# Optimization experiments

Measured on AMD Instinct MI355X. Metric: run time of the kernel, lower is better.

The kernel has to match this reference:

```python
import jax, jax.numpy as jnp
from jax import lax
import numpy as np

V, EMB, ELMO, WORD, H, B, R, L = 11322, 300, 1024, 512, 512, 32, 10, 20


def setup_inputs():
    key = jax.random.key(0)
    ks = jax.random.split(key, 24)

    def n(k, shape, s=0.02):
        return jax.random.normal(k, shape, dtype=jnp.float32) * s

    inp = {}
    inp["ques"] = jax.random.randint(ks[0], (B, R, L), 0, V)
    inp["hist"] = jax.random.randint(ks[1], (B, R, 2 * L), 0, V)
    inp["ques_len"] = jax.random.randint(ks[2], (B, R), 1, L + 1)
    inp["hist_len"] = jax.random.randint(ks[3], (B, R), 1, 2 * L + 1)
    inp["img_feat"] = n(ks[4], (B, 36, 2048), 1.0)
    inp["v_relations"] = n(ks[5], (B, 36, 36, 512), 1.0)
    inp["w_emb"] = n(ks[6], (V, EMB))          # GloVe/numberbatch table
    inp["elmo_emb"] = n(ks[7], (V, ELMO))      # frozen ELMo table
    inp["Wc"] = n(ks[8], (WORD, ELMO))         # embed_change Linear
    inp["bc"] = jnp.zeros((WORD,), jnp.float32)
    IN0 = EMB + WORD                            # LSTM layer-0 input size = 812
    names = ["q_Wih0", "q_Whh0", "q_b0", "q_Wih1", "q_Whh1", "q_b1",
             "h_Wih0", "h_Whh0", "h_b0", "h_Wih1", "h_Whh1", "h_b1"]
    shapes = [(4 * H, IN0), (4 * H, H), (4 * H,), (4 * H, H), (4 * H, H), (4 * H,)] * 2
    for i, (nm, sh) in enumerate(zip(names, shapes)):
        inp[nm] = n(ks[9 + i], sh, 0.04)
    return inp


def lstm_layer(x, Wih, Whh, b):
    # x: [N, T, In] -> all hidden states [N, T, H]; PyTorch gate order i,f,g,o
    N = x.shape[0]
    Hh = Whh.shape[1]
    xproj = jnp.einsum('nti,gi->ntg', x, Wih) + b  # [N, T, 4H]

    def step(carry, xp):
        h, c = carry
        gates = xp + h @ Whh.T
        i, f, g, o = jnp.split(gates, 4, axis=-1)
        c = jax.nn.sigmoid(f) * c + jax.nn.sigmoid(i) * jnp.tanh(g)
        h = jax.nn.sigmoid(o) * jnp.tanh(c)
        return (h, c), h

    h0 = jnp.zeros((N, Hh), x.dtype)
    _, hs = lax.scan(step, (h0, h0), jnp.swapaxes(xproj, 0, 1))
    return jnp.swapaxes(hs, 0, 1)


def encode(tokens, lens, w_emb, elmo_emb, Wc, bc, Wih0, Whh0, b0, Wih1, Whh1, b1):
    # Embedding lookup + elmo->word projection, 2-layer LSTM, take h at t = len-1
    Ntok = tokens.shape[0]
    emb = w_emb[tokens]                         # [N, T, 300]
    elmo = elmo_emb[tokens] @ Wc.T + bc         # [N, T, 512] (dropout off: eval)
    x = jnp.concatenate([emb, elmo], axis=-1)   # [N, T, 812]
    h1 = lstm_layer(x, Wih0, Whh0, b0)
    h2 = lstm_layer(h1, Wih1, Whh1, b1)
    return h2[jnp.arange(Ntok), lens - 1]       # DynamicRNN: last valid hidden


def reference(ques, hist, ques_len, hist_len, img_feat, v_relations, w_emb, elmo_emb, Wc, bc,
              q_Wih0, q_Whh0, q_b0, q_Wih1, q_Whh1, q_b1,
              h_Wih0, h_Whh0, h_b0, h_Wih1, h_Whh1, h_b1):
    Bq, Rr, Ll = ques.shape
    ques_embed = encode(ques.reshape(Bq * Rr, Ll), ques_len.reshape(-1),
                        w_emb, elmo_emb, Wc, bc,
                        q_Wih0, q_Whh0, q_b0, q_Wih1, q_Whh1, q_b1).reshape(Bq, Rr, -1)
    hist_embed = encode(hist.reshape(Bq * Rr, 2 * Ll), hist_len.reshape(-1),
                        w_emb, elmo_emb, Wc, bc,
                        h_Wih0, h_Whh0, h_b0, h_Wih1, h_Whh1, h_b1).reshape(Bq, Rr, -1)
    # Vectorized form of the Python double loop + pad_sequence:
    # f_history[b, i, j] = hist_embed[b, j] if j <= i else 0   -> [B, R, R, H]
    tri = jnp.tril(jnp.ones((Rr, Rr), hist_embed.dtype))
    f_history = hist_embed[:, None, :, :] * tri[None, :, :, None]
    # masks exactly as t_rel.abs().sum(-1).bool() on the broadcast tensors
    m = (jnp.abs(f_history).sum(-1) != 0)       # [B, R, R]
    # t_rel[b,i,j,k,:] = f_history[b,i,j,:] zeroed where tmp (=f_history[b,i,k]) is zero
    t_rel = f_history[:, :, :, None, :] * m[:, :, None, :, None]
    tmp = f_history[:, :, None, :, :] * m[:, :, :, None, None]
    text_rel = jnp.concatenate([t_rel, tmp], axis=-1)  # [B, R, R, R, 2H]
    return ques_embed, text_rel
```

## Files before the change

### kernel.cpp

```cpp
#include <hip/hip_runtime.h>
#include <math.h>

#define NSEQ 320
#define HDIM 512
#define G4   2048
#define EMBD 300
#define ELMOD 1024
#define XPAD 832

typedef __attribute__((ext_vector_type(8))) short bf16x8;
typedef __attribute__((ext_vector_type(4))) float f32x4;
typedef unsigned short ushort_t;

__device__ __forceinline__ float sigmoidf_(float x) { return 1.0f / (1.0f + expf(-x)); }

__device__ __forceinline__ ushort_t f2bf(float f) {
    unsigned u = __float_as_uint(f);
    u = (u + 0x7FFFu + ((u >> 16) & 1u)) >> 16;
    return (ushort_t)u;
}
__device__ __forceinline__ float bf2f(ushort_t u) {
    return __uint_as_float(((unsigned)u) << 16);
}
__device__ __forceinline__ unsigned pack2(float a, float b) {
    return (unsigned)f2bf(a) | ((unsigned)f2bf(b) << 16);
}

__global__ __launch_bounds__(256) void conv_bf16_kernel(
    const float* __restrict__ src, int srcCols,
    ushort_t* __restrict__ dst, int dstStride, int dstOff,
    int fillCols)
{
    int c = blockIdx.x * 256 + threadIdx.x;
    int r = blockIdx.y;
    if (c >= fillCols) return;
    float v = (c < srcCols) ? src[(size_t)r * srcCols + c] : 0.0f;
    dst[(size_t)r * dstStride + dstOff + c] = f2bf(v);
}

__global__ __launch_bounds__(128) void emb_gather_kernel(
    const int* __restrict__ tok, const float* __restrict__ w_emb,
    ushort_t* __restrict__ Xb)
{
    int n = blockIdx.x;
    int t = threadIdx.x;
    ushort_t* dst = Xb + (size_t)n * XPAD;
    if (t < 75) {
        const float4* src = (const float4*)(w_emb + (size_t)tok[n] * EMBD);
        float4 v = src[t];
        dst[4*t+0] = f2bf(v.x); dst[4*t+1] = f2bf(v.y);
        dst[4*t+2] = f2bf(v.z); dst[4*t+3] = f2bf(v.w);
    } else if (t >= 108) {
        dst[812 + (t - 108)] = 0;
    }
}

__global__ __launch_bounds__(256) void gemm_ff_kernel(
    const ushort_t* __restrict__ Ab, const float* __restrict__ Af,
    const int* __restrict__ tok, int strideA,
    const ushort_t* __restrict__ W, const float* __restrict__ bias,
    ushort_t* __restrict__ C, int strideC, int K)
{
    __shared__ ushort_t As[64 * 40];
    __shared__ ushort_t Bs[64 * 40];
    const int m0 = blockIdx.y * 64;
    const int n0 = blockIdx.x * 64;
    const int tid = threadIdx.x;
    const int r  = tid >> 2;
    const int kq = (tid & 3) << 3;

    const ushort_t* arow_b = nullptr;
    const float*    arow_f = nullptr;
    if (Af) arow_f = Af + (size_t)tok[m0 + r] * strideA + kq;
    else    arow_b = Ab + (size_t)(m0 + r) * strideA + kq;
    const ushort_t* brow = W + (size_t)(n0 + r) * K + kq;

    const int lane = tid & 63;
    const int w = tid >> 6;
    const int wm = w & 1, wn = w >> 1;
    const int kc = (lane >> 4) << 3;

    f32x4 acc[2][2];
    #pragma unroll
    for (int f = 0; f < 2; ++f)
        #pragma unroll
        for (int g = 0; g < 2; ++g)
            acc[f][g] = (f32x4){0.f, 0.f, 0.f, 0.f};

    for (int k0 = 0; k0 < K; k0 += 32) {
        if (Af) {
            float4 v0 = ((const float4*)(arow_f + k0))[0];
            float4 v1 = ((const float4*)(arow_f + k0))[1];
            uint4 p; p.x = pack2(v0.x, v0.y); p.y = pack2(v0.z, v0.w);
            p.z = pack2(v1.x, v1.y); p.w = pack2(v1.z, v1.w);
            *(uint4*)&As[r*40 + kq] = p;
        } else {
            *(uint4*)&As[r*40 + kq] = *(const uint4*)(arow_b + k0);
        }
        *(uint4*)&Bs[r*40 + kq] = *(const uint4*)(brow + k0);
        __syncthreads();
        bf16x8 af[2], bfr[2];
        #pragma unroll
        for (int f = 0; f < 2; ++f)
            af[f] = *(const bf16x8*)&As[(wm*32 + f*16 + (lane & 15))*40 + kc];
        #pragma unroll
        for (int g = 0; g < 2; ++g)
            bfr[g] = *(const bf16x8*)&Bs[(wn*32 + g*16 + (lane & 15))*40 + kc];
        #pragma unroll
        for (int f = 0; f < 2; ++f)
            #pragma unroll
            for (int g = 0; g < 2; ++g)
                acc[f][g] = __builtin_amdgcn_mfma_f32_16x16x32_bf16(af[f], bfr[g], acc[f][g], 0, 0, 0);
        __syncthreads();
    }

    #pragma unroll
    for (int f = 0; f < 2; ++f) {
        #pragma unroll
        for (int g = 0; g < 2; ++g) {
            int col = n0 + wn*32 + g*16 + (lane & 15);
            float bv = bias[col];
            #pragma unroll
            for (int i = 0; i < 4; ++i) {
                int row = m0 + wm*32 + f*16 + ((lane >> 4) << 2) + i;
                C[(size_t)row * strideC + col] = f2bf(acc[f][g][i] + bv);
            }
        }
    }
}

struct Cell {
    const ushort_t* A;
    const ushort_t* B;
    const ushort_t* xp;
    const float* bias;
    float* c;
    ushort_t* hA;
    ushort_t* hB;
    float* hlast;
    const int* lens;
    int t, K, strideHA, xpRowStride;
};
struct CellPack { Cell cells[4]; };

__global__ __launch_bounds__(256) void lstm_superstep_kernel(CellPack P)
{
    const Cell cl = P.cells[blockIdx.z];
    const int j0 = blockIdx.x * 16;
    const int n0 = blockIdx.y * 64;
    __shared__ ushort_t As[64 * 40];
    __shared__ ushort_t Bs[64 * 40];
    __shared__ float Gt[64][68];

    const int tid = threadIdx.x;
    const int r  = tid >> 2;
    const int kq = (tid & 3) << 3;
    const int K = cl.K;

    const ushort_t* arow = cl.A + (size_t)(n0 + r) * K + kq;
    const ushort_t* brow = cl.B + (size_t)((r >> 4) * HDIM + j0 + (r & 15)) * K + kq;

    const int lane = tid & 63;
    const int w = tid >> 6;
    const int wm = w & 1, wn = w >> 1;
    const int kc = (lane >> 4) << 3;

    f32x4 acc[2][2];
    #pragma unroll
    for (int f = 0; f < 2; ++f)
        #pragma unroll
        for (int g = 0; g < 2; ++g)
            acc[f][g] = (f32x4){0.f, 0.f, 0.f, 0.f};

    for (int k0 = 0; k0 < K; k0 += 32) {
        *(uint4*)&As[r*40 + kq] = *(const uint4*)(arow + k0);
        *(uint4*)&Bs[r*40 + kq] = *(const uint4*)(brow + k0);
        __syncthreads();
        bf16x8 af[2], bfr[2];
        #pragma unroll
        for (int f = 0; f < 2; ++f)
            af[f] = *(const bf16x8*)&As[(wm*32 + f*16 + (lane & 15))*40 + kc];
        #pragma unroll
        for (int g = 0; g < 2; ++g)
            bfr[g] = *(const bf16x8*)&Bs[(wn*32 + g*16 + (lane & 15))*40 + kc];
        #pragma unroll
        for (int f = 0; f < 2; ++f)
            #pragma unroll
            for (int g = 0; g < 2; ++g)
                acc[f][g] = __builtin_amdgcn_mfma_f32_16x16x32_bf16(af[f], bfr[g], acc[f][g], 0, 0, 0);
        __syncthreads();
    }

    #pragma unroll
    for (int f = 0; f < 2; ++f)
        #pragma unroll
        for (int g = 0; g < 2; ++g)
            #pragma unroll
            for (int i = 0; i < 4; ++i)
                Gt[wm*32 + f*16 + ((lane >> 4) << 2) + i][wn*32 + g*16 + (lane & 15)] = acc[f][g][i];
    __syncthreads();

    #pragma unroll
    for (int q = 0; q < 4; ++q) {
        int p = tid + q * 256;
        int nl = p >> 4, jj = p & 15;
        int n = n0 + nl, j = j0 + jj;
        float gi = Gt[nl][jj],      gf = Gt[nl][16 + jj];
        float gg = Gt[nl][32 + jj], go = Gt[nl][48 + jj];
        if (cl.xp) {
            const ushort_t* xr = cl.xp + (size_t)n * cl.xpRowStride;
            gi += bf2f(xr[j]);          gf += bf2f(xr[HDIM + j]);
            gg += bf2f(xr[2*HDIM + j]); go += bf2f(xr[3*HDIM + j]);
        } else {
            gi += cl.bias[j];          gf += cl.bias[HDIM + j];
            gg += cl.bias[2*HDIM + j]; go += cl.bias[3*HDIM + j];
        }
        size_t ix = (size_t)n * HDIM + j;
        float c = cl.c[ix];
        c = sigmoidf_(gf) * c + sigmoidf_(gi) * tanhf(gg);
        float h = sigmoidf_(go) * tanhf(c);
        cl.c[ix] = c;
        cl.hA[(size_t)n * cl.strideHA + j] = f2bf(h);
        if (cl.hB) cl.hB[(size_t)n * 1024 + j] = f2bf(h);
        if (cl.hlast && (cl.lens[n] - 1 == cl.t)) cl.hlast[ix] = h;
    }
}

__global__ __launch_bounds__(64) void nz_kernel(
    const float* __restrict__ he, int* __restrict__ nz)
{
    int rr = blockIdx.x;
    int lane = threadIdx.x;
    const float* row = he + (size_t)rr * HDIM;
    bool any = false;
    for (int k = lane; k < HDIM; k += 64) any |= (row[k] != 0.0f);
    unsigned long long b = __ballot(any);
    if (lane == 0) nz[rr] = (b != 0ull) ? 1 : 0;
}

__global__ __launch_bounds__(256) void expand_kernel(
    const float* __restrict__ he, const int* __restrict__ nz,
    float* __restrict__ out)
{
    int blk = blockIdx.x;
    int k = blk % 10;
    int j = (blk / 10) % 10;
    int i = (blk / 100) % 10;
    int b = blk / 1000;
    int tid = threadIdx.x;
    float4* o = (float4*)(out + (size_t)blk * 1024);
    float4 z; z.x = z.y = z.z = z.w = 0.0f;
    if (tid < 128) {
        bool m = (j <= i) && (k <= i) && (nz[b*10 + k] != 0);
        float4 v = m ? ((const float4*)(he + (size_t)(b*10 + j) * HDIM))[tid] : z;
        o[tid] = v;
    } else {
        int c = tid - 128;
        bool m = (k <= i) && (j <= i) && (nz[b*10 + j] != 0);
        float4 v = m ? ((const float4*)(he + (size_t)(b*10 + k) * HDIM))[c] : z;
        o[128 + c] = v;
    }
}

extern "C" void kernel_launch(void* const* d_in, const int* in_sizes, int n_in,
                              void* d_out, int out_size, void* d_ws, size_t ws_size,
                              hipStream_t stream)
{
    (void)in_sizes; (void)n_in; (void)out_size; (void)ws_size;
    const int* ques     = (const int*)d_in[0];
    const int* hist     = (const int*)d_in[1];
    const int* ques_len = (const int*)d_in[2];
    const int* hist_len = (const int*)d_in[3];
    const float* w_emb  = (const float*)d_in[6];
    const float* elmo   = (const float*)d_in[7];
    const float* Wc     = (const float*)d_in[8];
    const float* bc     = (const float*)d_in[9];

    char* ws = (char*)d_ws;
    size_t off = 0;
    auto alloc = [&](size_t bytes) { char* p = ws + off; off += (bytes + 15) & ~(size_t)15; return p; };
    ushort_t* XP0bf   = (ushort_t*)alloc((size_t)19200 * G4 * 2);
    ushort_t* Xb      = (ushort_t*)alloc((size_t)19200 * XPAD * 2);
    ushort_t* Wcb     = (ushort_t*)alloc((size_t)HDIM * ELMOD * 2);
    ushort_t* Wih0b[2], *Whh0b[2], *Wcat[2];
    for (int s = 0; s < 2; ++s) {
        Wih0b[s] = (ushort_t*)alloc((size_t)G4 * XPAD * 2);
        Whh0b[s] = (ushort_t*)alloc((size_t)G4 * HDIM * 2);
        Wcat[s]  = (ushort_t*)alloc((size_t)G4 * ELMOD * 2);
    }
    char* state_base = ws + off;
    ushort_t* h0buf[2][2];
    ushort_t* acat[2][2];
    float* cbuf[2][2];
    for (int s = 0; s < 2; ++s)
        for (int p = 0; p < 2; ++p) h0buf[s][p] = (ushort_t*)alloc((size_t)NSEQ * HDIM * 2);
    for (int s = 0; s < 2; ++s)
        for (int p = 0; p < 2; ++p) acat[s][p] = (ushort_t*)alloc((size_t)NSEQ * ELMOD * 2);
    for (int s = 0; s < 2; ++s)
        for (int l = 0; l < 2; ++l) cbuf[s][l] = (float*)alloc((size_t)NSEQ * HDIM * 4);
    size_t state_bytes = (ws + off) - state_base;
    float* he = (float*)alloc((size_t)NSEQ * HDIM * 4);
    int* nzb  = (int*)alloc(NSEQ * 4);

    float* out = (float*)d_out;
    float* ques_embed = out;
    float* text_rel   = out + (size_t)NSEQ * HDIM;

    const int rowoff[2] = {0, 6400};
    const int TT[2] = {20, 40};
    const int* toks[2] = {ques, hist};
    const int* lens[2] = {ques_len, hist_len};

    conv_bf16_kernel<<<dim3(4, HDIM), 256, 0, stream>>>(Wc, ELMOD, Wcb, ELMOD, 0, ELMOD);
    for (int s = 0; s < 2; ++s) {
        const float* Wih0 = (const float*)d_in[10 + 6*s];
        const float* Whh0 = (const float*)d_in[11 + 6*s];
        const float* Wih1 = (const float*)d_in[13 + 6*s];
        const float* Whh1 = (const float*)d_in[14 + 6*s];
        conv_bf16_kernel<<<dim3(4, G4), 256, 0, stream>>>(Wih0, 812, Wih0b[s], XPAD, 0, XPAD);
        conv_bf16_kernel<<<dim3(2, G4), 256, 0, stream>>>(Whh0, HDIM, Whh0b[s], HDIM, 0, HDIM);
        conv_bf16_kernel<<<dim3(2, G4), 256, 0, stream>>>(Wih1, HDIM, Wcat[s], ELMOD, 0, HDIM);
        conv_bf16_kernel<<<dim3(2, G4), 256, 0, stream>>>(Whh1, HDIM, Wcat[s], ELMOD, HDIM, HDIM);
    }

    for (int s = 0; s < 2; ++s) {
        int Ntok = NSEQ * TT[s];
        ushort_t* XbS = Xb + (size_t)rowoff[s] * XPAD;
        emb_gather_kernel<<<Ntok, 128, 0, stream>>>(toks[s], w_emb, XbS);
        gemm_ff_kernel<<<dim3(HDIM/64, Ntok/64), 256, 0, stream>>>(
            nullptr, elmo, toks[s], ELMOD, Wcb, bc, XbS + EMBD, XPAD, ELMOD);
        const float* b0 = (const float*)d_in[12 + 6*s];
        gemm_ff_kernel<<<dim3(G4/64, Ntok/64), 256, 0, stream>>>(
            XbS, nullptr, nullptr, XPAD, Wih0b[s], b0,
            XP0bf + (size_t)rowoff[s] * G4, G4, XPAD);
    }

    hipMemsetAsync(state_base, 0, state_bytes, stream);

    for (int ss = 0; ss <= 40; ++ss) {
        int par = ss & 1;
        CellPack P;
        int nc = 0;
        for (int s = 0; s < 2; ++s) {
            int T = TT[s];
            const float* b1 = (const float*)d_in[15 + 6*s];
            if (ss < T) {
                Cell& c = P.cells[nc++];
                c.A = h0buf[s][par]; c.B = Whh0b[s];
                c.xp = XP0bf + ((size_t)rowoff[s] + ss) * G4;
                c.xpRowStride = T * G4;
                c.bias = nullptr;
                c.c = cbuf[s][0];
                c.hA = h0buf[s][par ^ 1]; c.strideHA = HDIM;
                c.hB = acat[s][par ^ 1];
                c.hlast = nullptr; c.lens = lens[s];
                c.t = ss; c.K = HDIM;
            }
            if (ss >= 1 && ss <= T) {
                Cell& c = P.cells[nc++];
                c.A = acat[s][par]; c.B = Wcat[s];
                c.xp = nullptr; c.xpRowStride = 0;
                c.bias = b1;
                c.c = cbuf[s][1];
                c.hA = acat[s][par ^ 1] + HDIM; c.strideHA = ELMOD;
                c.hB = nullptr;
                c.hlast = s ? he : ques_embed; c.lens = lens[s];
                c.t = ss - 1; c.K = ELMOD;
            }
        }
        if (nc == 0) continue;
        lstm_superstep_kernel<<<dim3(HDIM/16, NSEQ/64, nc), 256, 0, stream>>>(P);
    }

    nz_kernel<<<NSEQ, 64, 0, stream>>>(he, nzb);
    expand_kernel<<<32000, 256, 0, stream>>>(he, nzb, text_rel);
}
```

Before: 1.192 ms.

## Replace per-timestep LSTM launches with a persistent kernel and grid barriers

Replaces the 41 per-superstep LSTM launches with one persistent kernel of 256 blocks, one group of 64 blocks per (sequence, layer) cell. The two cells of each sequence are synchronised between steps by an atomic-counter spin barrier. Cell state stays in registers, the A and B operands are loaded straight from global memory into registers with double buffering instead of going through LDS, and gate columns are arranged so each lane's i/f/g/o values are exchanged with shuffles. The aim is to remove launch overhead and the c-state round-trips to memory. In exchange it relies on all blocks being co-resident, and the spin loop has a timeout that could break correctness if it ever fires.

New measurement: 1.896 ms. 59.0% more time.

```diff
diff --git a/kernel.cpp b/kernel.cpp
--- a/kernel.cpp
+++ b/kernel.cpp
@@ -129,101 +129,141 @@
     }
 }
 
-struct Cell {
-    const ushort_t* A;
+struct PCell {
+    const ushort_t* A0; const ushort_t* A1;
     const ushort_t* B;
     const ushort_t* xp;
     const float* bias;
-    float* c;
-    ushort_t* hA;
-    ushort_t* hB;
+    ushort_t* O0; ushort_t* O1;
     float* hlast;
     const int* lens;
-    int t, K, strideHA, xpRowStride;
+    int K, T, layer;
 };
-struct CellPack { Cell cells[4]; };
-
-__global__ __launch_bounds__(256) void lstm_superstep_kernel(CellPack P)
-{
-    const Cell cl = P.cells[blockIdx.z];
-    const int j0 = blockIdx.x * 16;
-    const int n0 = blockIdx.y * 64;
-    __shared__ ushort_t As[64 * 40];
-    __shared__ ushort_t Bs[64 * 40];
-    __shared__ float Gt[64][68];
-
-    const int tid = threadIdx.x;
-    const int r  = tid >> 2;
-    const int kq = (tid & 3) << 3;
-    const int K = cl.K;
-
-    const ushort_t* arow = cl.A + (size_t)(n0 + r) * K + kq;
-    const ushort_t* brow = cl.B + (size_t)((r >> 4) * HDIM + j0 + (r & 15)) * K + kq;
-
+struct PPack { PCell cell[4]; };
+
+__global__ __launch_bounds__(256) void lstm_persist_kernel(PPack P, int* ctrs)
+{
+    const int cellId = blockIdx.x >> 6;
+    const int blk    = blockIdx.x & 63;
+    const PCell c = P.cell[cellId];
+    int* ctr = ctrs + (cellId >> 1) * 32;
+
+    const int tid  = threadIdx.x;
+    const int w    = tid >> 6;
     const int lane = tid & 63;
-    const int w = tid >> 6;
-    const int wm = w & 1, wn = w >> 1;
-    const int kc = (lane >> 4) << 3;
-
-    f32x4 acc[2][2];
+    const int cc   = lane & 15;
+    const int half = cc >> 3;
+    const int jj   = cc & 7;
+    const int kg   = lane >> 4;
+    const int j0   = blk * 8;
+    const int K    = c.K;
+    const int T    = c.T;
+    const int NK   = K >> 5;
+
+    int aoff[5];
     #pragma unroll
-    for (int f = 0; f < 2; ++f)
-        #pragma unroll
-        for (int g = 0; g < 2; ++g)
-            acc[f][g] = (f32x4){0.f, 0.f, 0.f, 0.f};
-
-    for (int k0 = 0; k0 < K; k0 += 32) {
-        *(uint4*)&As[r*40 + kq] = *(const uint4*)(arow + k0);
-        *(uint4*)&Bs[r*40 + kq] = *(const uint4*)(brow + k0);
-        __syncthreads();
-        bf16x8 af[2], bfr[2];
-        #pragma unroll
-        for (int f = 0; f < 2; ++f)
-            af[f] = *(const bf16x8*)&As[(wm*32 + f*16 + (lane & 15))*40 + kc];
-        #pragma unroll
-        for (int g = 0; g < 2; ++g)
-            bfr[g] = *(const bf16x8*)&Bs[(wn*32 + g*16 + (lane & 15))*40 + kc];
-        #pragma unroll
-        for (int f = 0; f < 2; ++f)
+    for (int q = 0; q < 5; ++q)
+        aoff[q] = ((w*5 + q)*16 + cc) * 1024 + kg*8;
+    const ushort_t* bptr0 = c.B + (size_t)((0*2 + half)*HDIM + j0 + jj) * K + kg*8;
+    const ushort_t* bptr1 = c.B + (size_t)((1*2 + half)*HDIM + j0 + jj) * K + kg*8;
+    const int x0col = half*HDIM + j0 + jj;
+    const int x1col = 1024 + x0col;
+    float bias0 = 0.f, bias1 = 0.f;
+    if (c.bias) { bias0 = c.bias[x0col]; bias1 = c.bias[x1col]; }
+    int lr[5][4];
+    #pragma unroll
+    for (int q = 0; q < 5; ++q)
+        #pragma unroll
+        for (int i = 0; i < 4; ++i)
+            lr[q][i] = c.lens[(w*5+q)*16 + kg*4 + i];
+
+    float creg[5][4];
+    #pragma unroll
+    for (int q = 0; q < 5; ++q)
+        #pragma unroll
+        for (int i = 0; i < 4; ++i) creg[q][i] = 0.f;
+
+#define LOADA(buf, kk) { _Pragma("unroll") \
+    for (int q = 0; q < 5; ++q) buf[q] = *(const uint4*)(Ab + aoff[q] + (kk)*32); }
+#define LOADB(buf, kk) { buf[0] = *(const uint4*)(bptr0 + (size_t)(kk)*32); \
+                         buf[1] = *(const uint4*)(bptr1 + (size_t)(kk)*32); }
+#define MF(ab, bb) { _Pragma("unroll") \
+    for (int q = 0; q < 5; ++q) { \
+        acc[q][0] = __builtin_amdgcn_mfma_f32_16x16x32_bf16(*(bf16x8*)&ab[q], *(bf16x8*)&bb[0], acc[q][0], 0, 0, 0); \
+        acc[q][1] = __builtin_amdgcn_mfma_f32_16x16x32_bf16(*(bf16x8*)&ab[q], *(bf16x8*)&bb[1], acc[q][1], 0, 0, 0); } }
+
+    for (int ss = 0; ss <= T; ++ss) {
+        const int par = ss & 1;
+        const bool active = c.layer ? (ss >= 1) : (ss < T);
+        if (active) {
+            const int t = c.layer ? (ss - 1) : ss;
+            const ushort_t* Ab = par ? c.A1 : c.A0;
+            ushort_t* Ob       = par ? c.O0 : c.O1;
+
+            f32x4 acc[5][2];
             #pragma unroll
-            for (int g = 0; g < 2; ++g)
-                acc[f][g] = __builtin_amdgcn_mfma_f32_16x16x32_bf16(af[f], bfr[g], acc[f][g], 0, 0, 0);
-        __syncthreads();
-    }
-
-    #pragma unroll
-    for (int f = 0; f < 2; ++f)
-        #pragma unroll
-        for (int g = 0; g < 2; ++g)
+            for (int q = 0; q < 5; ++q) {
+                acc[q][0] = (f32x4){0.f, 0.f, 0.f, 0.f};
+                acc[q][1] = (f32x4){0.f, 0.f, 0.f, 0.f};
+            }
+            uint4 aE[5], aO[5], bE2[2], bO2[2];
+            LOADA(aE, 0); LOADB(bE2, 0);
+            for (int kk = 0; kk < NK; kk += 2) {
+                if (kk + 1 < NK) { LOADA(aO, kk+1); LOADB(bO2, kk+1); }
+                MF(aE, bE2);
+                if (kk + 2 < NK) { LOADA(aE, kk+2); LOADB(bE2, kk+2); }
+                if (kk + 1 < NK) MF(aO, bO2);
+            }
+
             #pragma unroll
-            for (int i = 0; i < 4; ++i)
-                Gt[wm*32 + f*16 + ((lane >> 4) << 2) + i][wn*32 + g*16 + (lane & 15)] = acc[f][g][i];
-    __syncthreads();
-
-    #pragma unroll
-    for (int q = 0; q < 4; ++q) {
-        int p = tid + q * 256;
-        int nl = p >> 4, jj = p & 15;
-        int n = n0 + nl, j = j0 + jj;
-        float gi = Gt[nl][jj],      gf = Gt[nl][16 + jj];
-        float gg = Gt[nl][32 + jj], go = Gt[nl][48 + jj];
-        if (cl.xp) {
-            const ushort_t* xr = cl.xp + (size_t)n * cl.xpRowStride;
-            gi += bf2f(xr[j]);          gf += bf2f(xr[HDIM + j]);
-            gg += bf2f(xr[2*HDIM + j]); go += bf2f(xr[3*HDIM + j]);
-        } else {
-            gi += cl.bias[j];          gf += cl.bias[HDIM + j];
-            gg += cl.bias[2*HDIM + j]; go += cl.bias[3*HDIM + j];
+            for (int q = 0; q < 5; ++q) {
+                #pragma unroll
+                for (int i = 0; i < 4; ++i) {
+                    const int n = (w*5+q)*16 + kg*4 + i;
+                    float v0 = acc[q][0][i], v1 = acc[q][1][i];
+                    if (c.xp) {
+                        const ushort_t* xr = c.xp + ((size_t)n * T + t) * G4;
+                        v0 += bf2f(xr[x0col]); v1 += bf2f(xr[x1col]);
+                    } else {
+                        v0 += bias0; v1 += bias1;
+                    }
+                    float u0 = __shfl_xor(v0, 8);
+                    float u1 = __shfl_xor(v1, 8);
+                    float gi = half ? u0 : v0;
+                    float gf = half ? v0 : u0;
+                    float gg = half ? u1 : v1;
+                    float go = half ? v1 : u1;
+                    float cn = sigmoidf_(gf) * creg[q][i] + sigmoidf_(gi) * tanhf(gg);
+                    creg[q][i] = cn;
+                    float h = sigmoidf_(go) * tanhf(cn);
+                    unsigned hb = (unsigned)f2bf(h);
+                    unsigned pb = (unsigned)__shfl_xor((int)hb, 1);
+                    if (half == 0 && (jj & 1) == 0)
+                        *(unsigned*)(Ob + (size_t)n * 1024 + j0 + jj) = hb | (pb << 16);
+                    if (c.hlast && half == 0 && t == lr[q][i] - 1)
+                        c.hlast[(size_t)n * HDIM + j0 + jj] = h;
+                }
+            }
         }
-        size_t ix = (size_t)n * HDIM + j;
-        float c = cl.c[ix];
-        c = sigmoidf_(gf) * c + sigmoidf_(gi) * tanhf(gg);
-        float h = sigmoidf_(go) * tanhf(c);
-        cl.c[ix] = c;
-        cl.hA[(size_t)n * cl.strideHA + j] = f2bf(h);
-        if (cl.hB) cl.hB[(size_t)n * 1024 + j] = f2bf(h);
-        if (cl.hlast && (cl.lens[n] - 1 == cl.t)) cl.hlast[ix] = h;
-    }
+        if (ss < T) {
+            __syncthreads();
+            if (tid == 0) {
+                __builtin_amdgcn_fence(__ATOMIC_RELEASE, "agent");
+                __hip_atomic_fetch_add(ctr, 1, __ATOMIC_RELAXED, __HIP_MEMORY_SCOPE_AGENT);
+                const int tgt = 128 * (ss + 1);
+                int spins = 0;
+                while (__hip_atomic_load(ctr, __ATOMIC_RELAXED, __HIP_MEMORY_SCOPE_AGENT) < tgt) {
+                    __builtin_amdgcn_s_sleep(2);
+                    if (++spins > (1 << 18)) break;
+                }
+                __builtin_amdgcn_fence(__ATOMIC_ACQUIRE, "agent");
+            }
+            __syncthreads();
+        }
+    }
+#undef LOADA
+#undef LOADB
+#undef MF
 }
 
 __global__ __launch_bounds__(64) void nz_kernel(
@@ -278,26 +318,22 @@
 
     char* ws = (char*)d_ws;
     size_t off = 0;
-    auto alloc = [&](size_t bytes) { char* p = ws + off; off += (bytes + 15) & ~(size_t)15; return p; };
-    ushort_t* XP0bf   = (ushort_t*)alloc((size_t)19200 * G4 * 2);
-    ushort_t* Xb      = (ushort_t*)alloc((size_t)19200 * XPAD * 2);
-    ushort_t* Wcb     = (ushort_t*)alloc((size_t)HDIM * ELMOD * 2);
-    ushort_t* Wih0b[2], *Whh0b[2], *Wcat[2];
+    auto alloc = [&](size_t bytes) { char* p = ws + off; off += (bytes + 255) & ~(size_t)255; return p; };
+    ushort_t* XP0bf = (ushort_t*)alloc((size_t)19200 * G4 * 2);
+    ushort_t* Xb    = (ushort_t*)alloc((size_t)19200 * XPAD * 2);
+    ushort_t* Wcb   = (ushort_t*)alloc((size_t)HDIM * ELMOD * 2);
+    ushort_t *Wih0b[2], *Whh0b[2], *Wcat[2];
     for (int s = 0; s < 2; ++s) {
         Wih0b[s] = (ushort_t*)alloc((size_t)G4 * XPAD * 2);
         Whh0b[s] = (ushort_t*)alloc((size_t)G4 * HDIM * 2);
         Wcat[s]  = (ushort_t*)alloc((size_t)G4 * ELMOD * 2);
     }
     char* state_base = ws + off;
-    ushort_t* h0buf[2][2];
     ushort_t* acat[2][2];
-    float* cbuf[2][2];
     for (int s = 0; s < 2; ++s)
-        for (int p = 0; p < 2; ++p) h0buf[s][p] = (ushort_t*)alloc((size_t)NSEQ * HDIM * 2);
-    for (int s = 0; s < 2; ++s)
-        for (int p = 0; p < 2; ++p) acat[s][p] = (ushort_t*)alloc((size_t)NSEQ * ELMOD * 2);
-    for (int s = 0; s < 2; ++s)
-        for (int l = 0; l < 2; ++l) cbuf[s][l] = (float*)alloc((size_t)NSEQ * HDIM * 4);
+        for (int p = 0; p < 2; ++p)
+            acat[s][p] = (ushort_t*)alloc((size_t)NSEQ * ELMOD * 2);
+    int* ctrs = (int*)alloc(256);
     size_t state_bytes = (ws + off) - state_base;
     float* he = (float*)alloc((size_t)NSEQ * HDIM * 4);
     int* nzb  = (int*)alloc(NSEQ * 4);
@@ -309,7 +345,7 @@
     const int rowoff[2] = {0, 6400};
     const int TT[2] = {20, 40};
     const int* toks[2] = {ques, hist};
-    const int* lens[2] = {ques_len, hist_len};
+    const int* lensp[2] = {ques_len, hist_len};
 
     conv_bf16_kernel<<<dim3(4, HDIM), 256, 0, stream>>>(Wc, ELMOD, Wcb, ELMOD, 0, ELMOD);
     for (int s = 0; s < 2; ++s) {
@@ -337,40 +373,27 @@
 
     hipMemsetAsync(state_base, 0, state_bytes, stream);
 
-    for (int ss = 0; ss <= 40; ++ss) {
-        int par = ss & 1;
-        CellPack P;
-        int nc = 0;
-        for (int s = 0; s < 2; ++s) {
-            int T = TT[s];
-            const float* b1 = (const float*)d_in[15 + 6*s];
-            if (ss < T) {
-                Cell& c = P.cells[nc++];
-                c.A = h0buf[s][par]; c.B = Whh0b[s];
-                c.xp = XP0bf + ((size_t)rowoff[s] + ss) * G4;
-                c.xpRowStride = T * G4;
-                c.bias = nullptr;
-                c.c = cbuf[s][0];
-                c.hA = h0buf[s][par ^ 1]; c.strideHA = HDIM;
-                c.hB = acat[s][par ^ 1];
-                c.hlast = nullptr; c.lens = lens[s];
-                c.t = ss; c.K = HDIM;
-            }
-            if (ss >= 1 && ss <= T) {
-                Cell& c = P.cells[nc++];
-                c.A = acat[s][par]; c.B = Wcat[s];
-                c.xp = nullptr; c.xpRowStride = 0;
-                c.bias = b1;
-                c.c = cbuf[s][1];
-                c.hA = acat[s][par ^ 1] + HDIM; c.strideHA = ELMOD;
-                c.hB = nullptr;
-                c.hlast = s ? he : ques_embed; c.lens = lens[s];
-                c.t = ss - 1; c.K = ELMOD;
-            }
-        }
-        if (nc == 0) continue;
-        lstm_superstep_kernel<<<dim3(HDIM/16, NSEQ/64, nc), 256, 0, stream>>>(P);
-    }
+    PPack P;
+    for (int s = 0; s < 2; ++s) {
+        const float* b1 = (const float*)d_in[15 + 6*s];
+        PCell& c0 = P.cell[s*2 + 0];
+        c0.A0 = acat[s][0]; c0.A1 = acat[s][1];
+        c0.B  = Whh0b[s];
+        c0.xp = XP0bf + (size_t)rowoff[s] * G4;
+        c0.bias = nullptr;
+        c0.O0 = acat[s][0]; c0.O1 = acat[s][1];
+        c0.hlast = nullptr; c0.lens = lensp[s];
+        c0.K = HDIM; c0.T = TT[s]; c0.layer = 0;
+        PCell& c1 = P.cell[s*2 + 1];
+        c1.A0 = acat[s][0]; c1.A1 = acat[s][1];
+        c1.B  = Wcat[s];
+        c1.xp = nullptr; c1.bias = b1;
+        c1.O0 = acat[s][0] + HDIM; c1.O1 = acat[s][1] + HDIM;
+        c1.hlast = s ? he : ques_embed;
+        c1.lens = lensp[s];
+        c1.K = ELMOD; c1.T = TT[s]; c1.layer = 1;
+    }
+    lstm_persist_kernel<<<256, 256, 0, stream>>>(P, ctrs);
 
     nz_kernel<<<NSEQ, 64, 0, stream>>>(he, nzb);
     expand_kernel<<<32000, 256, 0, stream>>>(he, nzb, text_rel);
```
